# Kernel tuning notes

Measured on AMD Instinct MI355X. Metric: run time of the kernel, lower is better.

Reference implementation:

```python
import jax, jax.numpy as jnp
import numpy as np

B, D, L = 32, 64, 8192
K = 512
COMMITMENT_COST = 0.1


def setup_inputs() -> dict:
    key = jax.random.key(0)
    k1, k2 = jax.random.split(key)
    x = jax.random.normal(k1, (B, D, L), dtype=jnp.float32)
    # Embedding initialized uniform(-1/K, 1/K) as in the torch module
    weight = jax.random.uniform(k2, (K, D), dtype=jnp.float32, minval=-1.0 / K, maxval=1.0 / K)
    return {"x": x, "weight": weight}


def reference(x, weight):
    # x: [B, D, L] -> inputs: [B, L, D]
    inputs = jnp.transpose(x, (0, 2, 1))
    flat = inputs.reshape(-1, D)  # [N, D]
    # Squared L2 distances to codebook: [N, K]
    distances = (
        jnp.sum(flat * flat, axis=1, keepdims=True)
        + jnp.sum(weight * weight, axis=1)
        - 2.0 * flat @ weight.T
    )
    encoding_indices = jnp.argmin(distances, axis=1)  # [N]
    # Gather quantized vectors (equivalent to one-hot @ weight)
    quantized = weight[encoding_indices].reshape(inputs.shape)  # [B, L, D]
    e_latent_loss = jnp.mean((jax.lax.stop_gradient(quantized) - inputs) ** 2)
    q_latent_loss = jnp.mean((quantized - jax.lax.stop_gradient(inputs)) ** 2)
    loss = q_latent_loss + COMMITMENT_COST * e_latent_loss
    # Straight-through estimator
    quantized_st = inputs + jax.lax.stop_gradient(quantized - inputs)
    out = jnp.transpose(quantized_st, (0, 2, 1))  # [B, D, L]
    # perplexity = number of unique codes used (jit-friendly via bincount)
    perplexity = jnp.sum(jnp.bincount(encoding_indices, length=K) > 0)
    return (out, loss, perplexity, weight, encoding_indices[:, None])
```

## Files before the change

### kernel.cpp

```cpp
#include <hip/hip_runtime.h>
#include <math.h>

#define BB 32
#define DD 64
#define LL 8192
#define KK 512
#define NN (BB*LL)

#define OUT0_SZ  (BB*DD*LL)
#define LOSS_OFF (OUT0_SZ)
#define PERP_OFF (OUT0_SZ + 1)
#define W_OFF    (OUT0_SZ + 2)
#define IDX_OFF  (W_OFF + KK*DD)

#define WS_TVEC 0
#define WS_HIST 512
#define WS_LACC 1024
#define WS_WPH  1032
#define WS_WPL  (1032 + 16384)

typedef __attribute__((ext_vector_type(4))) float f32x4;
typedef __attribute__((ext_vector_type(8))) short s16x8;
typedef unsigned long long u64;

#define WINDOW 1e-4f

__device__ __forceinline__ unsigned short f2bf(float f) {
  unsigned int u = __float_as_uint(f);
  return (unsigned short)((u + 0x7FFFu + ((u >> 16) & 1u)) >> 16);
}
__device__ __forceinline__ float bf2f(unsigned short s) {
  return __uint_as_float(((unsigned int)s) << 16);
}
__device__ __forceinline__ u64 shflx64(u64 v, int m) {
  unsigned lo = __shfl_xor((unsigned)v, m);
  unsigned hi = __shfl_xor((unsigned)(v >> 32), m);
  return ((u64)hi << 32) | lo;
}
__device__ __forceinline__ unsigned fenc(float f) {
  unsigned u = __float_as_uint(f);
  return (u & 0x80000000u) ? ~u : (u | 0x80000000u);
}
__device__ __forceinline__ float fdec(unsigned e) {
  return __uint_as_float((e & 0x80000000u) ? (e ^ 0x80000000u) : ~e);
}

__global__ void vq_init(const float* __restrict__ w, float* __restrict__ ws,
                        float* __restrict__ dout) {
#pragma clang fp contract(off)
  int t = blockIdx.x * blockDim.x + threadIdx.x;
  if (t < KK) {
    const float* wr = w + t * DD;
    float r[8];
#pragma unroll
    for (int j = 0; j < 8; j++) { float v = wr[j]; r[j] = v * v; }
#pragma unroll
    for (int blk = 8; blk < 64; blk += 8) {
#pragma unroll
      for (int j = 0; j < 8; j++) { float v = wr[blk + j]; float a = v * v; r[j] = r[j] + a; }
    }
    ws[WS_TVEC + t] = ((r[0] + r[1]) + (r[2] + r[3])) + ((r[4] + r[5]) + (r[6] + r[7]));
    ((int*)ws)[WS_HIST + t] = 0;
  }
  if (t == 0) ws[WS_LACC] = 0.0f;

  {
    int j    = t & 7;
    int lane = (t >> 3) & 63;
    int ks   = (t >> 9) & 1;
    int ct   = t >> 10;
    int code = ct * 16 + (lane & 15);
    int d    = ks * 32 + ((lane >> 4) << 3) + j;
    float v  = w[code * DD + d];
    unsigned short h = f2bf(v);
    unsigned short l = f2bf(v - bf2f(h));
    ((unsigned short*)(ws + WS_WPH))[((ct * 2 + ks) * 64 + lane) * 8 + j] = h;
    ((unsigned short*)(ws + WS_WPL))[((ct * 2 + ks) * 64 + lane) * 8 + j] = l;
  }

  if (t < KK * DD / 2) {
    ((float2*)(dout + W_OFF))[t] = ((const float2*)w)[t];
  }
}

__launch_bounds__(256, 2)
__global__ void vq_main(const float* __restrict__ x, const float* __restrict__ w,
                        const float* __restrict__ ws, float* __restrict__ dout) {
#pragma clang fp contract(off)
  __shared__ uint4 xs_lds[4][64][8];
  __shared__ float t_lds[KK];
  __shared__ u64   g_lds[256];
  __shared__ unsigned short cand[256][4];
  __shared__ int   ccnt[256];
  __shared__ unsigned char flags[KK];

  const float* tvec = ws + WS_TVEC;
  const s16x8* wph8 = (const s16x8*)(ws + WS_WPH);
  const s16x8* wpl8 = (const s16x8*)(ws + WS_WPL);
  int* hist = (int*)ws + WS_HIST;
  float* lacc = (float*)ws + WS_LACC;

  const int tid  = threadIdx.x;
  const int lane = tid & 63;
  const int wv   = tid >> 6;
  const int res  = lane & 15;

  for (int e = tid; e < KK; e += 256) { t_lds[e] = tvec[e]; flags[e] = 0; }
  ccnt[tid] = 0;

  const int n = blockIdx.x * 256 + wv * 64 + lane;
  const int b = n >> 13, l = n & 8191;
  const float* px = x + (size_t)b * DD * LL + l;

  s16x8 afh[4][2], afl[4][2];
  {
    float xv[64];
#pragma unroll
    for (int i = 0; i < 64; i++) xv[i] = px[(size_t)i * LL];

#pragma unroll
    for (int blk = 0; blk < 8; blk++) {
      unsigned ph[4];
#pragma unroll
      for (int q = 0; q < 4; q++) {
        float v0 = xv[blk * 8 + 2 * q], v1 = xv[blk * 8 + 2 * q + 1];
        ph[q] = (unsigned)f2bf(v0) | ((unsigned)f2bf(v1) << 16);
      }
      int sw = blk ^ (lane & 7);
      uint4 vh; vh.x = ph[0]; vh.y = ph[1]; vh.z = ph[2]; vh.w = ph[3];
      xs_lds[wv][lane][sw] = vh;
    }
    __syncthreads();
    {
      const s16x8* xs8 = (const s16x8*)xs_lds;
#pragma unroll
      for (int t2 = 0; t2 < 4; t2++)
#pragma unroll
        for (int ks = 0; ks < 2; ks++) {
          int idx = (wv * 64 + t2 * 16 + (lane & 15)) * 8 + ((ks * 4 + (lane >> 4)) ^ (lane & 7));
          afh[t2][ks] = xs8[idx];
        }
    }
    __syncthreads();

#pragma unroll
    for (int blk = 0; blk < 8; blk++) {
      unsigned pl[4];
#pragma unroll
      for (int q = 0; q < 4; q++) {
        float v0 = xv[blk * 8 + 2 * q],     h0f = bf2f(f2bf(v0));
        float v1 = xv[blk * 8 + 2 * q + 1], h1f = bf2f(f2bf(v1));
        pl[q] = (unsigned)f2bf(v0 - h0f) | ((unsigned)f2bf(v1 - h1f) << 16);
      }
      int sw = blk ^ (lane & 7);
      uint4 vl; vl.x = pl[0]; vl.y = pl[1]; vl.z = pl[2]; vl.w = pl[3];
      xs_lds[wv][lane][sw] = vl;
    }
    __syncthreads();
    {
      const s16x8* xs8 = (const s16x8*)xs_lds;
#pragma unroll
      for (int t2 = 0; t2 < 4; t2++)
#pragma unroll
        for (int ks = 0; ks < 2; ks++) {
          int idx = (wv * 64 + t2 * 16 + (lane & 15)) * 8 + ((ks * 4 + (lane >> 4)) ^ (lane & 7));
          afl[t2][ks] = xs8[idx];
        }
    }
  }

  float d1[4][4], d2[4][4]; int k1[4][4];
#pragma unroll
  for (int t2 = 0; t2 < 4; t2++)
#pragma unroll
    for (int r = 0; r < 4; r++) { d1[t2][r] = INFINITY; d2[t2][r] = INFINITY; k1[t2][r] = 0; }

  s16x8 bh0 = wph8[lane], bh1 = wph8[64 + lane];
  s16x8 bl0 = wpl8[lane], bl1 = wpl8[64 + lane];
  float tc = t_lds[res];

#pragma clang loop unroll(disable)
  for (int ct = 0; ct < 32; ct++) {
    int cn = (ct + 1) & 31;
    s16x8 nh0 = wph8[cn * 128 + lane],      nh1 = wph8[cn * 128 + 64 + lane];
    s16x8 nl0 = wpl8[cn * 128 + lane],      nl1 = wpl8[cn * 128 + 64 + lane];
    float ntc = t_lds[cn * 16 + res];

#pragma unroll
    for (int t2 = 0; t2 < 4; t2++) {
      f32x4 acc = {0.f, 0.f, 0.f, 0.f};
      acc = __builtin_amdgcn_mfma_f32_16x16x32_bf16(afl[t2][0], bh0, acc, 0, 0, 0);
      acc = __builtin_amdgcn_mfma_f32_16x16x32_bf16(afl[t2][1], bh1, acc, 0, 0, 0);
      acc = __builtin_amdgcn_mfma_f32_16x16x32_bf16(afh[t2][0], bl0, acc, 0, 0, 0);
      acc = __builtin_amdgcn_mfma_f32_16x16x32_bf16(afh[t2][1], bl1, acc, 0, 0, 0);
      acc = __builtin_amdgcn_mfma_f32_16x16x32_bf16(afh[t2][0], bh0, acc, 0, 0, 0);
      acc = __builtin_amdgcn_mfma_f32_16x16x32_bf16(afh[t2][1], bh1, acc, 0, 0, 0);
#pragma unroll
      for (int r = 0; r < 4; r++) {
        float dap = fmaf(-2.0f, acc[r], tc);
        bool c1 = dap < d1[t2][r];
        bool c2 = dap < d2[t2][r];
        d2[t2][r] = c1 ? d1[t2][r] : (c2 ? dap : d2[t2][r]);
        d1[t2][r] = c1 ? dap : d1[t2][r];
        k1[t2][r] = c1 ? ct : k1[t2][r];
      }
    }
    bh0 = nh0; bh1 = nh1; bl0 = nl0; bl1 = nl1; tc = ntc;
  }

  __builtin_amdgcn_sched_barrier(0);
  float xr[64];
#pragma unroll
  for (int i = 0; i < 64; i++) xr[i] = px[(size_t)i * LL];

  u64 gmin[4][4];
#pragma unroll
  for (int t2 = 0; t2 < 4; t2++)
#pragma unroll
    for (int r = 0; r < 4; r++) {
      u64 pk = (((u64)fenc(d1[t2][r])) << 32) | (u64)(k1[t2][r] * 16 + res);
      u64 q1 = shflx64(pk, 1); pk = pk < q1 ? pk : q1;
      u64 q2 = shflx64(pk, 2); pk = pk < q2 ? pk : q2;
      u64 q4 = shflx64(pk, 4); pk = pk < q4 ? pk : q4;
      u64 q8 = shflx64(pk, 8); pk = pk < q8 ? pk : q8;
      gmin[t2][r] = pk;
    }

#pragma unroll
  for (int t2 = 0; t2 < 4; t2++)
#pragma unroll
    for (int r = 0; r < 4; r++) {
      int row = wv * 64 + t2 * 16 + ((lane >> 4) << 2) + r;
      if (res == 0) g_lds[row] = gmin[t2][r];
      float thr = fdec((unsigned)(gmin[t2][r] >> 32)) + WINDOW;
      bool in1 = d1[t2][r] <= thr;
      bool in2 = d2[t2][r] <= thr;
      if (in1) { int p = atomicAdd(&ccnt[row], 1); if (p < 4) cand[row][p] = (unsigned short)(k1[t2][r] * 16 + res); }
      if (in2) { int p = atomicAdd(&ccnt[row], 1); if (p < 4) cand[row][p] = (unsigned short)(512 + res); }
    }
  __syncthreads();

  int kwin;
  {
    int row = wv * 64 + lane;
    int cnt = ccnt[row];
    if (cnt <= 1) {
      kwin = (int)(g_lds[row] & 0x1FFu);
    } else {
      float s;
      {
        float r[8];
#pragma unroll
        for (int j = 0; j < 8; j++) r[j] = xr[j] * xr[j];
#pragma unroll
        for (int blk = 8; blk < 64; blk += 8)
#pragma unroll
          for (int j = 0; j < 8; j++) { float a = xr[blk + j] * xr[blk + j]; r[j] = r[j] + a; }
        s = ((r[0] + r[1]) + (r[2] + r[3])) + ((r[4] + r[5]) + (r[6] + r[7]));
      }
      u64 best = ~0ULL;
      auto evalExact = [&](int c) {
        const float4* wr = (const float4*)(w + c * DD);
        float gg = 0.0f;
#pragma unroll
        for (int i = 0; i < 16; i++) {
          float4 wq = wr[i];
          gg = fmaf(xr[4 * i + 0], wq.x, gg); gg = fmaf(xr[4 * i + 1], wq.y, gg);
          gg = fmaf(xr[4 * i + 2], wq.z, gg); gg = fmaf(xr[4 * i + 3], wq.w, gg);
        }
        float de = fmaf(-2.0f, gg, s + t_lds[c]);
        u64 pk = (((u64)__float_as_uint(de)) << 32) | (u64)c;
        if (pk < best) best = pk;
      };
      if (cnt > 4) {
        for (int c = 0; c < KK; c++) evalExact(c);
      } else {
        for (int i = 0; i < cnt; i++) {
          int c = cand[row][i];
          if (c < 512) evalExact(c);
          else { int c0 = c - 512; for (int jj = 0; jj < 32; jj++) evalExact(jj * 16 + c0); }
        }
      }
      kwin = (int)(best & 0x1FFu);
    }
  }

  float ls = 0.0f;
  {
    float* o = dout + (size_t)b * DD * LL + l;
    const float4* wr = (const float4*)(w + kwin * DD);
#pragma unroll
    for (int i = 0; i < 16; i++) {
      float4 v = wr[i];
      o[(size_t)(4 * i + 0) * LL] = v.x; o[(size_t)(4 * i + 1) * LL] = v.y;
      o[(size_t)(4 * i + 2) * LL] = v.z; o[(size_t)(4 * i + 3) * LL] = v.w;
      float df;
      df = v.x - xr[4 * i + 0]; ls = fmaf(df, df, ls);
      df = v.y - xr[4 * i + 1]; ls = fmaf(df, df, ls);
      df = v.z - xr[4 * i + 2]; ls = fmaf(df, df, ls);
      df = v.w - xr[4 * i + 3]; ls = fmaf(df, df, ls);
    }
  }
  dout[IDX_OFF + n] = (float)kwin;
  flags[kwin] = 1;

#pragma unroll
  for (int o = 32; o > 0; o >>= 1) ls += __shfl_down(ls, o);
  if ((tid & 63) == 0) atomicAdd(lacc, ls);

  __syncthreads();
  for (int e = tid; e < KK; e += 256)
    if (flags[e]) atomicOr(&hist[e], 1);
}

__global__ void vq_final(const float* __restrict__ ws, float* __restrict__ dout) {
  __shared__ int red[512];
  const int* hist = (const int*)ws + WS_HIST;
  int tid = threadIdx.x;
  red[tid] = (hist[tid] != 0) ? 1 : 0;
  __syncthreads();
  for (int sx = 256; sx > 0; sx >>= 1) {
    if (tid < sx) red[tid] += red[tid + sx];
    __syncthreads();
  }
  if (tid == 0) {
    dout[PERP_OFF] = (float)red[0];
    float m = ws[WS_LACC] / 16777216.0f;
    dout[LOSS_OFF] = m + 0.1f * m;
  }
}

extern "C" void kernel_launch(void* const* d_in, const int* in_sizes, int n_in,
                              void* d_out, int out_size, void* d_ws, size_t ws_size,
                              hipStream_t stream) {
  const float* x = (const float*)d_in[0];
  const float* w = (const float*)d_in[1];
  float* dout = (float*)d_out;
  float* ws = (float*)d_ws;

  vq_init<<<128, 256, 0, stream>>>(w, ws, dout);
  vq_main<<<NN / 256, 256, 0, stream>>>(x, w, ws, dout);
  vq_final<<<1, 512, 0, stream>>>(ws, dout);
}
```

Baseline: 236.8 us.

## Pack distance and index into one uint, defer x reload, fold final reduction

Biases distances by a constant so they stay positive, then packs the truncated float bits together with the codebook-tile index into a single unsigned word. This turns the top-2 tracking into plain integer min/max operations with fewer registers. The fp32 x reload is moved after candidate selection to shorten register live ranges. The separate final kernel is removed: the last block, found with an atomic counter, computes perplexity and loss. Truncating the low mantissa bits may change which codes tie, though the exact-recheck window is meant to absorb this.

```diff
diff --git a/kernel.cpp b/kernel.cpp
--- a/kernel.cpp
+++ b/kernel.cpp
@@ -16,6 +16,7 @@
 #define WS_TVEC 0
 #define WS_HIST 512
 #define WS_LACC 1024
+#define WS_CTR  1025
 #define WS_WPH  1032
 #define WS_WPL  (1032 + 16384)
 
@@ -24,6 +25,7 @@
 typedef unsigned long long u64;
 
 #define WINDOW 1e-4f
+#define DBIAS  4.0f
 
 __device__ __forceinline__ unsigned short f2bf(float f) {
   unsigned int u = __float_as_uint(f);
@@ -36,13 +38,6 @@
   unsigned lo = __shfl_xor((unsigned)v, m);
   unsigned hi = __shfl_xor((unsigned)(v >> 32), m);
   return ((u64)hi << 32) | lo;
-}
-__device__ __forceinline__ unsigned fenc(float f) {
-  unsigned u = __float_as_uint(f);
-  return (u & 0x80000000u) ? ~u : (u | 0x80000000u);
-}
-__device__ __forceinline__ float fdec(unsigned e) {
-  return __uint_as_float((e & 0x80000000u) ? (e ^ 0x80000000u) : ~e);
 }
 
 __global__ void vq_init(const float* __restrict__ w, float* __restrict__ ws,
@@ -62,7 +57,7 @@
     ws[WS_TVEC + t] = ((r[0] + r[1]) + (r[2] + r[3])) + ((r[4] + r[5]) + (r[6] + r[7]));
     ((int*)ws)[WS_HIST + t] = 0;
   }
-  if (t == 0) ws[WS_LACC] = 0.0f;
+  if (t == 0) { ws[WS_LACC] = 0.0f; ((int*)ws)[WS_CTR] = 0; }
 
   {
     int j    = t & 7;
@@ -93,12 +88,14 @@
   __shared__ unsigned short cand[256][4];
   __shared__ int   ccnt[256];
   __shared__ unsigned char flags[KK];
+  __shared__ int   lastblk;
 
   const float* tvec = ws + WS_TVEC;
   const s16x8* wph8 = (const s16x8*)(ws + WS_WPH);
   const s16x8* wpl8 = (const s16x8*)(ws + WS_WPL);
   int* hist = (int*)ws + WS_HIST;
   float* lacc = (float*)ws + WS_LACC;
+  int* ctr = (int*)ws + WS_CTR;
 
   const int tid  = threadIdx.x;
   const int lane = tid & 63;
@@ -169,22 +166,23 @@
     }
   }
 
-  float d1[4][4], d2[4][4]; int k1[4][4];
+  unsigned pk1[4][4], pk2[4][4];
 #pragma unroll
   for (int t2 = 0; t2 < 4; t2++)
 #pragma unroll
-    for (int r = 0; r < 4; r++) { d1[t2][r] = INFINITY; d2[t2][r] = INFINITY; k1[t2][r] = 0; }
+    for (int r = 0; r < 4; r++) { pk1[t2][r] = 0xFFFFFFFFu; pk2[t2][r] = 0xFFFFFFFFu; }
+  const unsigned MASKQ = 0xFFFFFFE0u;
 
   s16x8 bh0 = wph8[lane], bh1 = wph8[64 + lane];
   s16x8 bl0 = wpl8[lane], bl1 = wpl8[64 + lane];
-  float tc = t_lds[res];
+  float tcb = t_lds[res] + DBIAS;
 
 #pragma clang loop unroll(disable)
   for (int ct = 0; ct < 32; ct++) {
     int cn = (ct + 1) & 31;
     s16x8 nh0 = wph8[cn * 128 + lane],      nh1 = wph8[cn * 128 + 64 + lane];
     s16x8 nl0 = wpl8[cn * 128 + lane],      nl1 = wpl8[cn * 128 + 64 + lane];
-    float ntc = t_lds[cn * 16 + res];
+    float ntcb = t_lds[cn * 16 + res] + DBIAS;
 
 #pragma unroll
     for (int t2 = 0; t2 < 4; t2++) {
@@ -197,28 +195,23 @@
       acc = __builtin_amdgcn_mfma_f32_16x16x32_bf16(afh[t2][1], bh1, acc, 0, 0, 0);
 #pragma unroll
       for (int r = 0; r < 4; r++) {
-        float dap = fmaf(-2.0f, acc[r], tc);
-        bool c1 = dap < d1[t2][r];
-        bool c2 = dap < d2[t2][r];
-        d2[t2][r] = c1 ? d1[t2][r] : (c2 ? dap : d2[t2][r]);
-        d1[t2][r] = c1 ? dap : d1[t2][r];
-        k1[t2][r] = c1 ? ct : k1[t2][r];
-      }
-    }
-    bh0 = nh0; bh1 = nh1; bl0 = nl0; bl1 = nl1; tc = ntc;
-  }
-
-  __builtin_amdgcn_sched_barrier(0);
-  float xr[64];
-#pragma unroll
-  for (int i = 0; i < 64; i++) xr[i] = px[(size_t)i * LL];
+        float dap = fmaf(-2.0f, acc[r], tcb);
+        unsigned pkd = (__float_as_uint(dap) & MASKQ) | (unsigned)ct;
+        unsigned mx = pk1[t2][r] > pkd ? pk1[t2][r] : pkd;
+        pk2[t2][r] = pk2[t2][r] < mx ? pk2[t2][r] : mx;
+        pk1[t2][r] = pk1[t2][r] < pkd ? pk1[t2][r] : pkd;
+      }
+    }
+    bh0 = nh0; bh1 = nh1; bl0 = nl0; bl1 = nl1; tcb = ntcb;
+  }
 
   u64 gmin[4][4];
 #pragma unroll
   for (int t2 = 0; t2 < 4; t2++)
 #pragma unroll
     for (int r = 0; r < 4; r++) {
-      u64 pk = (((u64)fenc(d1[t2][r])) << 32) | (u64)(k1[t2][r] * 16 + res);
+      unsigned k9 = ((pk1[t2][r] & 31u) << 4) | (unsigned)res;
+      u64 pk = (((u64)(pk1[t2][r] & MASKQ)) << 32) | (u64)k9;
       u64 q1 = shflx64(pk, 1); pk = pk < q1 ? pk : q1;
       u64 q2 = shflx64(pk, 2); pk = pk < q2 ? pk : q2;
       u64 q4 = shflx64(pk, 4); pk = pk < q4 ? pk : q4;
@@ -232,15 +225,20 @@
     for (int r = 0; r < 4; r++) {
       int row = wv * 64 + t2 * 16 + ((lane >> 4) << 2) + r;
       if (res == 0) g_lds[row] = gmin[t2][r];
-      float thr = fdec((unsigned)(gmin[t2][r] >> 32)) + WINDOW;
-      bool in1 = d1[t2][r] <= thr;
-      bool in2 = d2[t2][r] <= thr;
-      if (in1) { int p = atomicAdd(&ccnt[row], 1); if (p < 4) cand[row][p] = (unsigned short)(k1[t2][r] * 16 + res); }
+      float thr = __uint_as_float((unsigned)(gmin[t2][r] >> 32)) + WINDOW;
+      float d1f = __uint_as_float(pk1[t2][r] & MASKQ);
+      float d2f = __uint_as_float(pk2[t2][r] & MASKQ);
+      bool in1 = d1f <= thr;
+      bool in2 = d2f <= thr;
+      if (in1) { int p = atomicAdd(&ccnt[row], 1); if (p < 4) cand[row][p] = (unsigned short)(((pk1[t2][r] & 31u) << 4) | res); }
       if (in2) { int p = atomicAdd(&ccnt[row], 1); if (p < 4) cand[row][p] = (unsigned short)(512 + res); }
     }
   __syncthreads();
 
   int kwin;
+  float xr[64];
+#pragma unroll
+  for (int i = 0; i < 64; i++) xr[i] = px[(size_t)i * LL];
   {
     int row = wv * 64 + lane;
     int cnt = ccnt[row];
@@ -311,22 +309,27 @@
   __syncthreads();
   for (int e = tid; e < KK; e += 256)
     if (flags[e]) atomicOr(&hist[e], 1);
-}
-
-__global__ void vq_final(const float* __restrict__ ws, float* __restrict__ dout) {
-  __shared__ int red[512];
-  const int* hist = (const int*)ws + WS_HIST;
-  int tid = threadIdx.x;
-  red[tid] = (hist[tid] != 0) ? 1 : 0;
+
+  __threadfence();
+  if (tid == 0) {
+    int old = atomicAdd(ctr, 1);
+    lastblk = (old == (int)gridDim.x - 1) ? 1 : 0;
+  }
   __syncthreads();
-  for (int sx = 256; sx > 0; sx >>= 1) {
-    if (tid < sx) red[tid] += red[tid + sx];
+  if (lastblk) {
+    int c0 = (atomicOr(&hist[tid], 0) != 0) ? 1 : 0;
+    int c1 = (atomicOr(&hist[tid + 256], 0) != 0) ? 1 : 0;
+    ccnt[tid] = c0 + c1;
     __syncthreads();
-  }
-  if (tid == 0) {
-    dout[PERP_OFF] = (float)red[0];
-    float m = ws[WS_LACC] / 16777216.0f;
-    dout[LOSS_OFF] = m + 0.1f * m;
+    for (int sx = 128; sx > 0; sx >>= 1) {
+      if (tid < sx) ccnt[tid] += ccnt[tid + sx];
+      __syncthreads();
+    }
+    if (tid == 0) {
+      dout[PERP_OFF] = (float)ccnt[0];
+      float m = atomicAdd(lacc, 0.0f) / 16777216.0f;
+      dout[LOSS_OFF] = m + 0.1f * m;
+    }
   }
 }
 
@@ -340,5 +343,4 @@
 
   vq_init<<<128, 256, 0, stream>>>(w, ws, dout);
   vq_main<<<NN / 256, 256, 0, stream>>>(x, w, ws, dout);
-  vq_final<<<1, 512, 0, stream>>>(ws, dout);
-}
+}
```

New measurement: 337.9 us. +42.7%, slower.
